# Kernel optimization log

Measured on AMD Instinct MI355X. Metric: run time of the kernel, lower is better.

Reference implementation:

```python
import jax, jax.numpy as jnp
import numpy as np

H = 256  # hidden size
I = 2    # input size / output size


def setup_inputs() -> dict:
    key = jax.random.key(0)
    ks = jax.random.split(key, 11)
    s1 = 1.0 / np.sqrt(H)
    u = lambda k, shape: jax.random.uniform(k, shape, jnp.float32, -s1, s1)
    return {
        "inputs": jax.random.normal(ks[0], (512, 256, I), jnp.float32),
        "W_ih1": u(ks[1], (4 * H, I)),
        "W_hh1": u(ks[2], (4 * H, H)),
        "b_ih1": u(ks[3], (4 * H,)),
        "b_hh1": u(ks[4], (4 * H,)),
        "W_ih2": u(ks[5], (4 * H, H)),
        "W_hh2": u(ks[6], (4 * H, H)),
        "b_ih2": u(ks[7], (4 * H,)),
        "b_hh2": u(ks[8], (4 * H,)),
        "W_lin": u(ks[9], (I, H)),
        "b_lin": u(ks[10], (I,)),
    }


def _lstm_cell(x, h, c, W_ih, W_hh, b_ih, b_hh):
    # PyTorch LSTMCell gate order: i, f, g, o
    gates = x @ W_ih.T + b_ih + h @ W_hh.T + b_hh  # (B, 4H)
    i, f, g, o = jnp.split(gates, 4, axis=-1)
    c_new = jax.nn.sigmoid(f) * c + jax.nn.sigmoid(i) * jnp.tanh(g)
    h_new = jax.nn.sigmoid(o) * jnp.tanh(c_new)
    return h_new, c_new


def reference(inputs, W_ih1, W_hh1, b_ih1, b_hh1, W_ih2, W_hh2, b_ih2, b_hh2,
              W_lin, b_lin):
    B = inputs.shape[0]
    xs = jnp.transpose(inputs, (1, 0, 2))  # (T, B, I)
    zeros = jnp.zeros((B, H), inputs.dtype)
    carry0 = (zeros, zeros, zeros, zeros)

    def step(carry, x_t):
        h1, c1, h2, c2 = carry
        # NOTE: the original clones/masks x_t into lstm_input_t but never
        # uses it — the cell consumes raw input_t, so we do the same.
        h1, c1 = _lstm_cell(x_t, h1, c1, W_ih1, W_hh1, b_ih1, b_hh1)
        h2, c2 = _lstm_cell(h1, h2, c2, W_ih2, W_hh2, b_ih2, b_hh2)
        y = h2 @ W_lin.T + b_lin  # (B, I)
        return (h1, c1, h2, c2), y

    _, ys = jax.lax.scan(step, carry0, xs)  # ys: (T, B, I)
    return jnp.transpose(ys, (1, 0, 2))  # (B, T, I)
```

## Files before the change

kernel.cpp:

```cpp
#include <hip/hip_runtime.h>


typedef float vf2 __attribute__((ext_vector_type(2)));
typedef float v4f __attribute__((ext_vector_type(4)));
typedef _Float16 vh4 __attribute__((ext_vector_type(4)));
typedef _Float16 vh8 __attribute__((ext_vector_type(8)));

#define NT 512
#define TSTEPS 256
#define NSF 144
#define NVPF 32
#define NLPF 16
#define FRB 1024
#define VPBASE (1152 * FRB)
#define LPBASE (1408 * FRB)
#define FS 393216

__global__ void prep_kernel(const float* __restrict__ W_ih1,
                            const float* __restrict__ W_hh1,
                            const float* __restrict__ b_ih1,
                            const float* __restrict__ b_hh1,
                            const float* __restrict__ W_ih2,
                            const float* __restrict__ W_hh2,
                            const float* __restrict__ b_ih2,
                            const float* __restrict__ b_hh2,
                            void* __restrict__ ws) {
    const int stride = gridDim.x * blockDim.x;
    const int idx = blockIdx.x * blockDim.x + threadIdx.x;
    _Float16* wh = (_Float16*)ws;
    float* wf = (float*)ws;
    for (int e = idx; e < 786432; e += stride) {
        int kb = e >> 9;
        int lane = (e & 511) >> 3, jj = e & 7;
        int w, rt, kt, m;
        if (kb < 1152) {
            w = kb / 144; int f = kb % 144;
            if (f < 64)       { m = 0; rt = f >> 3;        kt = f & 7; }
            else if (f < 128) { m = 1; rt = (f - 64) >> 3; kt = f & 7; }
            else { int q = f - 128; m = 2; rt = q >> 1; kt = (q & 1) ? 5 : 0; }
        } else if (kb < 1408) {
            int p2 = kb - 1152; w = p2 >> 5; int p = p2 & 31;
            m = 2; rt = p >> 2; kt = 1 + (p & 3);
        } else {
            int k3 = kb - 1408; w = k3 >> 4; int q = k3 & 15;
            m = 2; rt = q >> 1; kt = 6 + (q & 1);
        }
        int row = w * 128 + rt * 16 + (lane & 15);
        int k   = kt * 32 + ((lane >> 4) << 3) + jj;
        float v = (m == 0) ? W_hh1[row * 256 + k]
                : (m == 1) ? W_ih2[row * 256 + k]
                           : W_hh2[row * 256 + k];
        wh[e] = (_Float16)v;
    }
    for (int j = idx; j < 1024; j += stride) {
        wf[FS + j]        = W_ih1[j * 2 + 0];
        wf[FS + 1024 + j] = W_ih1[j * 2 + 1];
        wf[FS + 2048 + j] = b_ih1[j] + b_hh1[j];
        wf[FS + 3072 + j] = b_ih2[j] + b_hh2[j];
    }
}

__device__ __forceinline__ float sig_(float v) {
    return 1.f / (1.f + __expf(-v));
}
__device__ __forceinline__ float tanh_(float v) {
    return 1.f - 2.f / (__expf(2.f * v) + 1.f);
}
__device__ __forceinline__ v4f mfma16(vh8 a, vh8 b, v4f c) {
    return __builtin_amdgcn_mfma_f32_16x16x32_f16(a, b, c, 0, 0, 0);
}

#define BARRIER() __asm__ volatile("s_waitcnt lgkmcnt(0)\ns_barrier" ::: "memory")

__global__ __launch_bounds__(NT, 2) void lstm_kernel(
    const float* __restrict__ x,
    const void* __restrict__ ws,
    const float* __restrict__ W_lin,
    const float* __restrict__ b_lin,
    float* __restrict__ out)
{
    __shared__ float g1buf[2][1024];
    __shared__ float g2buf[2][1024];
    __shared__ __align__(16) _Float16 h1s[2][256];
    __shared__ __align__(16) _Float16 h2s[2][256];
    __shared__ __align__(16) char lds_park[NLPF * 8 * FRB];

    const int tid = threadIdx.x;
    const int lane = tid & 63, w = tid >> 6;
    const int u = tid & 255, bu = tid >> 8;
    const int b0 = blockIdx.x * 2;
    const char* wstream = (const char*)ws;
    const float* wf = (const float*)ws;
    const int l16 = lane * 16;

    float wxa[4], wxb[4], b1c[4], b2c[4];
    #pragma unroll
    for (int g = 0; g < 4; ++g) {
        int r = g * 256 + u;
        wxa[g] = wf[FS + r];        wxb[g] = wf[FS + 1024 + r];
        b1c[g] = wf[FS + 2048 + r]; b2c[g] = wf[FS + 3072 + r];
    }

    const int ob = (w >> 1) & 1, oo = w & 1;
    const float wl0 = W_lin[oo * 256 + 4 * lane + 0];
    const float wl1 = W_lin[oo * 256 + 4 * lane + 1];
    const float wl2 = W_lin[oo * 256 + 4 * lane + 2];
    const float wl3 = W_lin[oo * 256 + 4 * lane + 3];
    const float blin = b_lin[oo];

    ((_Float16*)h1s)[tid] = (_Float16)0.f;
    ((_Float16*)h2s)[tid] = (_Float16)0.f;
    g1buf[0][tid] = 0.f; g1buf[0][512 + tid] = 0.f;
    g1buf[1][tid] = 0.f; g1buf[1][512 + tid] = 0.f;

    float c1 = 0.f, c2 = 0.f;

    for (int q = 0; q < NLPF; ++q) {
        *(vh8*)&lds_park[(((q << 3) + w) << 10) + l16] =
            *(const vh8*)(wstream + LPBASE + (((w << 4) + q) << 10) + l16);
    }

    vh8 wreg[NVPF];
    #pragma unroll
    for (int p = 0; p < NVPF; ++p) {
        union { vh8 v; float f[4]; } tpk;
        tpk.v = *(const vh8*)(wstream + VPBASE + ((w * NVPF + p) << 10) + l16);
        asm volatile("" : "+v"(tpk.f[0]), "+v"(tpk.f[1]),
                          "+v"(tpk.f[2]), "+v"(tpk.f[3]));
        wreg[p] = tpk.v;
    }

    const char* wbase = wstream + (size_t)w * (NSF * FRB);
    int sp = 0;
    vh8 B0, B1, B2, B3, B4, B5, B6, B7;
    auto LDA = [&](vh8& d) {
        d = *(const vh8*)(wbase + sp + l16);
        sp += FRB; if (sp == NSF * FRB) sp = 0;
    };
    LDA(B0); LDA(B1); LDA(B2); LDA(B3);
    LDA(B4); LDA(B5); LDA(B6); LDA(B7);

    auto bfrag = [&](const _Float16 (*hp)[256], int kt) -> vh8 {
        return *(const vh8*)&hp[lane & 1][kt * 32 + ((lane >> 4) << 3)];
    };

    const int bx = b0 + bu;
    vf2 xv = *(const vf2*)(x + (size_t)bx * 512);

    __syncthreads();

    #pragma unroll 1
    for (int t = 0; t < TSTEPS; ++t) {
        {
            float p0 = g1buf[bu][u]       + b1c[0] + wxa[0] * xv.x + wxb[0] * xv.y;
            float p1 = g1buf[bu][256 + u] + b1c[1] + wxa[1] * xv.x + wxb[1] * xv.y;
            float p2 = g1buf[bu][512 + u] + b1c[2] + wxa[2] * xv.x + wxb[2] * xv.y;
            float p3 = g1buf[bu][768 + u] + b1c[3] + wxa[3] * xv.x + wxb[3] * xv.y;
            c1 = sig_(p1) * c1 + sig_(p0) * tanh_(p2);
            h1s[bu][u] = (_Float16)(sig_(p3) * tanh_(c1));
        }
        {
            const int tn = (t + 1) & (TSTEPS - 1);
            xv = *(const vf2*)(x + (size_t)bx * 512 + tn * 2);
        }
        BARRIER();

        if (t > 0 && w < 4) {
            vh4 hv = *(const vh4*)&h2s[ob][4 * lane];
            float s = (float)hv.x * wl0 + (float)hv.y * wl1
                    + (float)hv.z * wl2 + (float)hv.w * wl3;
            #pragma unroll
            for (int m = 32; m >= 1; m >>= 1) s += __shfl_xor(s, m, 64);
            if (lane == 0)
                out[(size_t)(b0 + ob) * 512 + (t - 1) * 2 + oo] = s + blin;
        }

        #pragma unroll 1
        for (int rt = 0; rt < 8; ++rt) {
            v4f acc = {0.f, 0.f, 0.f, 0.f};
            acc = mfma16(B0, bfrag(h1s, 0), acc); LDA(B0);
            acc = mfma16(B1, bfrag(h1s, 1), acc); LDA(B1);
            acc = mfma16(B2, bfrag(h1s, 2), acc); LDA(B2);
            acc = mfma16(B3, bfrag(h1s, 3), acc); LDA(B3);
            acc = mfma16(B4, bfrag(h1s, 4), acc); LDA(B4);
            acc = mfma16(B5, bfrag(h1s, 5), acc); LDA(B5);
            acc = mfma16(B6, bfrag(h1s, 6), acc); LDA(B6);
            acc = mfma16(B7, bfrag(h1s, 7), acc); LDA(B7);
            if ((lane & 15) < 2)
                *(v4f*)&g1buf[lane & 15][w * 128 + rt * 16 + ((lane >> 4) << 2)] = acc;
        }

        #pragma unroll 1
        for (int rt = 0; rt < 8; ++rt) {
            v4f acc = {0.f, 0.f, 0.f, 0.f};
            acc = mfma16(B0, bfrag(h1s, 0), acc); LDA(B0);
            acc = mfma16(B1, bfrag(h1s, 1), acc); LDA(B1);
            acc = mfma16(B2, bfrag(h1s, 2), acc); LDA(B2);
            acc = mfma16(B3, bfrag(h1s, 3), acc); LDA(B3);
            acc = mfma16(B4, bfrag(h1s, 4), acc); LDA(B4);
            acc = mfma16(B5, bfrag(h1s, 5), acc); LDA(B5);
            acc = mfma16(B6, bfrag(h1s, 6), acc); LDA(B6);
            acc = mfma16(B7, bfrag(h1s, 7), acc); LDA(B7);
            if ((lane & 15) < 2)
                *(v4f*)&g2buf[lane & 15][w * 128 + rt * 16 + ((lane >> 4) << 2)] = acc;
        }

#define P2B(RT, BA, BB)                                                        \
        {                                                                      \
            v4f acc = {0.f, 0.f, 0.f, 0.f};                                    \
            if ((lane & 15) < 2)                                               \
                acc = *(const v4f*)&g2buf[lane & 15]                           \
                        [w * 128 + RT * 16 + ((lane >> 4) << 2)];              \
            acc = mfma16(BA, bfrag(h2s, 0), acc); LDA(BA);                     \
            acc = mfma16(wreg[RT * 4 + 0], bfrag(h2s, 1), acc);                \
            acc = mfma16(wreg[RT * 4 + 1], bfrag(h2s, 2), acc);                \
            acc = mfma16(wreg[RT * 4 + 2], bfrag(h2s, 3), acc);                \
            acc = mfma16(wreg[RT * 4 + 3], bfrag(h2s, 4), acc);                \
            acc = mfma16(BB, bfrag(h2s, 5), acc); LDA(BB);                     \
            {                                                                  \
                vh8 A6 = *(const vh8*)                                         \
                    &lds_park[((((RT * 2 + 0) << 3) + w) << 10) + l16];        \
                acc = mfma16(A6, bfrag(h2s, 6), acc);                          \
            }                                                                  \
            {                                                                  \
                vh8 A7 = *(const vh8*)                                         \
                    &lds_park[((((RT * 2 + 1) << 3) + w) << 10) + l16];        \
                acc = mfma16(A7, bfrag(h2s, 7), acc);                          \
            }                                                                  \
            if ((lane & 15) < 2)                                               \
                *(v4f*)&g2buf[lane & 15]                                       \
                    [w * 128 + RT * 16 + ((lane >> 4) << 2)] = acc;            \
        }
        P2B(0, B0, B1) P2B(1, B2, B3) P2B(2, B4, B5) P2B(3, B6, B7)
        P2B(4, B0, B1) P2B(5, B2, B3) P2B(6, B4, B5) P2B(7, B6, B7)
#undef P2B
        BARRIER();

        {
            float q0 = g2buf[bu][u]       + b2c[0];
            float q1 = g2buf[bu][256 + u] + b2c[1];
            float q2 = g2buf[bu][512 + u] + b2c[2];
            float q3 = g2buf[bu][768 + u] + b2c[3];
            c2 = sig_(q1) * c2 + sig_(q0) * tanh_(q2);
            h2s[bu][u] = (_Float16)(sig_(q3) * tanh_(c2));
        }
    }

    BARRIER();
    if (w < 4) {
        vh4 hv = *(const vh4*)&h2s[ob][4 * lane];
        float s = (float)hv.x * wl0 + (float)hv.y * wl1
                + (float)hv.z * wl2 + (float)hv.w * wl3;
        #pragma unroll
        for (int m = 32; m >= 1; m >>= 1) s += __shfl_xor(s, m, 64);
        if (lane == 0)
            out[(size_t)(b0 + ob) * 512 + 255 * 2 + oo] = s + blin;
    }
}

extern "C" void kernel_launch(void* const* d_in, const int* in_sizes, int n_in,
                              void* d_out, int out_size, void* d_ws, size_t ws_size,
                              hipStream_t stream) {
    const float* x     = (const float*)d_in[0];
    const float* W_ih1 = (const float*)d_in[1];
    const float* W_hh1 = (const float*)d_in[2];
    const float* b_ih1 = (const float*)d_in[3];
    const float* b_hh1 = (const float*)d_in[4];
    const float* W_ih2 = (const float*)d_in[5];
    const float* W_hh2 = (const float*)d_in[6];
    const float* b_ih2 = (const float*)d_in[7];
    const float* b_hh2 = (const float*)d_in[8];
    const float* W_lin = (const float*)d_in[9];
    const float* b_lin = (const float*)d_in[10];
    float* out = (float*)d_out;

    prep_kernel<<<256, 256, 0, stream>>>(W_ih1, W_hh1, b_ih1, b_hh1,
                                         W_ih2, W_hh2, b_ih2, b_hh2, d_ws);
    lstm_kernel<<<256, NT, 0, stream>>>(x, d_ws, W_lin, b_lin, out);
}
```

Baseline: 2.705 ms.

## Process four batch rows per block and rebalance weight residency between LDS and stream

Each block now handles four batch elements instead of two, with 128 blocks instead of 256. The same streamed weight fragments feed MFMAs over more batch columns, so global weight traffic per batch element is halved. To fit the larger gate and hidden buffers in LDS, the parked W_hh2 tile for kt=7 moves back into the global stream, so the per-step stream grows from 144 to 152 fragments. Each thread now runs two LSTM cell updates per layer, and only half as many blocks are launched, which may leave CUs idle.

```diff
diff --git a/kernel.cpp b/kernel.cpp
--- a/kernel.cpp
+++ b/kernel.cpp
@@ -8,12 +8,12 @@
 
 #define NT 512
 #define TSTEPS 256
-#define NSF 144
+#define NSF 152
 #define NVPF 32
-#define NLPF 16
+#define NLPF 8
 #define FRB 1024
-#define VPBASE (1152 * FRB)
-#define LPBASE (1408 * FRB)
+#define VPBASE (1216 * FRB)
+#define LPBASE (1472 * FRB)
 #define FS 393216
 
 __global__ void prep_kernel(const float* __restrict__ W_ih1,
@@ -33,17 +33,20 @@
         int kb = e >> 9;
         int lane = (e & 511) >> 3, jj = e & 7;
         int w, rt, kt, m;
-        if (kb < 1152) {
-            w = kb / 144; int f = kb % 144;
+        if (kb < 1216) {
+            w = kb / 152; int f = kb % 152;
             if (f < 64)       { m = 0; rt = f >> 3;        kt = f & 7; }
             else if (f < 128) { m = 1; rt = (f - 64) >> 3; kt = f & 7; }
-            else { int q = f - 128; m = 2; rt = q >> 1; kt = (q & 1) ? 5 : 0; }
-        } else if (kb < 1408) {
-            int p2 = kb - 1152; w = p2 >> 5; int p = p2 & 31;
+            else {
+                int q = f - 128; m = 2; rt = q / 3; int pos = q % 3;
+                kt = (pos == 0) ? 0 : (pos == 1) ? 5 : 7;
+            }
+        } else if (kb < 1472) {
+            int p2 = kb - 1216; w = p2 >> 5; int p = p2 & 31;
             m = 2; rt = p >> 2; kt = 1 + (p & 3);
         } else {
-            int k3 = kb - 1408; w = k3 >> 4; int q = k3 & 15;
-            m = 2; rt = q >> 1; kt = 6 + (q & 1);
+            int k3 = kb - 1472; w = k3 >> 3; int q = k3 & 7;
+            m = 2; rt = q; kt = 6;
         }
         int row = w * 128 + rt * 16 + (lane & 15);
         int k   = kt * 32 + ((lane >> 4) << 3) + jj;
@@ -79,16 +82,16 @@
     const float* __restrict__ b_lin,
     float* __restrict__ out)
 {
-    __shared__ float g1buf[2][1024];
-    __shared__ float g2buf[2][1024];
-    __shared__ __align__(16) _Float16 h1s[2][256];
-    __shared__ __align__(16) _Float16 h2s[2][256];
+    __shared__ float g1buf[4][1024];
+    __shared__ float g2buf[4][1024];
+    __shared__ __align__(16) _Float16 h1s[4][288];
+    __shared__ __align__(16) _Float16 h2s[4][288];
     __shared__ __align__(16) char lds_park[NLPF * 8 * FRB];
 
     const int tid = threadIdx.x;
     const int lane = tid & 63, w = tid >> 6;
     const int u = tid & 255, bu = tid >> 8;
-    const int b0 = blockIdx.x * 2;
+    const int b0 = blockIdx.x * 4;
     const char* wstream = (const char*)ws;
     const float* wf = (const float*)ws;
     const int l16 = lane * 16;
@@ -101,23 +104,24 @@
         b1c[g] = wf[FS + 2048 + r]; b2c[g] = wf[FS + 3072 + r];
     }
 
-    const int ob = (w >> 1) & 1, oo = w & 1;
+    const int ob = w >> 1, oo = w & 1;
     const float wl0 = W_lin[oo * 256 + 4 * lane + 0];
     const float wl1 = W_lin[oo * 256 + 4 * lane + 1];
     const float wl2 = W_lin[oo * 256 + 4 * lane + 2];
     const float wl3 = W_lin[oo * 256 + 4 * lane + 3];
     const float blin = b_lin[oo];
 
-    ((_Float16*)h1s)[tid] = (_Float16)0.f;
-    ((_Float16*)h2s)[tid] = (_Float16)0.f;
-    g1buf[0][tid] = 0.f; g1buf[0][512 + tid] = 0.f;
-    g1buf[1][tid] = 0.f; g1buf[1][512 + tid] = 0.f;
-
-    float c1 = 0.f, c2 = 0.f;
+    for (int i = tid; i < 4 * 288; i += NT) {
+        ((_Float16*)h1s)[i] = (_Float16)0.f;
+        ((_Float16*)h2s)[i] = (_Float16)0.f;
+    }
+    for (int i = tid; i < 4096; i += NT) ((float*)g1buf)[i] = 0.f;
+
+    float c1a = 0.f, c1b = 0.f, c2a = 0.f, c2b = 0.f;
 
     for (int q = 0; q < NLPF; ++q) {
         *(vh8*)&lds_park[(((q << 3) + w) << 10) + l16] =
-            *(const vh8*)(wstream + LPBASE + (((w << 4) + q) << 10) + l16);
+            *(const vh8*)(wstream + LPBASE + (((w << 3) + q) << 10) + l16);
     }
 
     vh8 wreg[NVPF];
@@ -140,32 +144,40 @@
     LDA(B0); LDA(B1); LDA(B2); LDA(B3);
     LDA(B4); LDA(B5); LDA(B6); LDA(B7);
 
-    auto bfrag = [&](const _Float16 (*hp)[256], int kt) -> vh8 {
-        return *(const vh8*)&hp[lane & 1][kt * 32 + ((lane >> 4) << 3)];
+    auto bfrag = [&](const _Float16 (*hp)[288], int kt) -> vh8 {
+        return *(const vh8*)&hp[lane & 3][kt * 32 + ((lane >> 4) << 3)];
     };
 
-    const int bx = b0 + bu;
-    vf2 xv = *(const vf2*)(x + (size_t)bx * 512);
+    const int bxa = b0 + bu, bxb = b0 + bu + 2;
+    vf2 xva = *(const vf2*)(x + (size_t)bxa * 512);
+    vf2 xvb = *(const vf2*)(x + (size_t)bxb * 512);
 
     __syncthreads();
 
     #pragma unroll 1
     for (int t = 0; t < TSTEPS; ++t) {
         {
-            float p0 = g1buf[bu][u]       + b1c[0] + wxa[0] * xv.x + wxb[0] * xv.y;
-            float p1 = g1buf[bu][256 + u] + b1c[1] + wxa[1] * xv.x + wxb[1] * xv.y;
-            float p2 = g1buf[bu][512 + u] + b1c[2] + wxa[2] * xv.x + wxb[2] * xv.y;
-            float p3 = g1buf[bu][768 + u] + b1c[3] + wxa[3] * xv.x + wxb[3] * xv.y;
-            c1 = sig_(p1) * c1 + sig_(p0) * tanh_(p2);
-            h1s[bu][u] = (_Float16)(sig_(p3) * tanh_(c1));
+            float p0 = g1buf[bu][u]       + b1c[0] + wxa[0] * xva.x + wxb[0] * xva.y;
+            float p1 = g1buf[bu][256 + u] + b1c[1] + wxa[1] * xva.x + wxb[1] * xva.y;
+            float p2 = g1buf[bu][512 + u] + b1c[2] + wxa[2] * xva.x + wxb[2] * xva.y;
+            float p3 = g1buf[bu][768 + u] + b1c[3] + wxa[3] * xva.x + wxb[3] * xva.y;
+            c1a = sig_(p1) * c1a + sig_(p0) * tanh_(p2);
+            h1s[bu][u] = (_Float16)(sig_(p3) * tanh_(c1a));
+            float q0 = g1buf[bu + 2][u]       + b1c[0] + wxa[0] * xvb.x + wxb[0] * xvb.y;
+            float q1 = g1buf[bu + 2][256 + u] + b1c[1] + wxa[1] * xvb.x + wxb[1] * xvb.y;
+            float q2 = g1buf[bu + 2][512 + u] + b1c[2] + wxa[2] * xvb.x + wxb[2] * xvb.y;
+            float q3 = g1buf[bu + 2][768 + u] + b1c[3] + wxa[3] * xvb.x + wxb[3] * xvb.y;
+            c1b = sig_(q1) * c1b + sig_(q0) * tanh_(q2);
+            h1s[bu + 2][u] = (_Float16)(sig_(q3) * tanh_(c1b));
         }
         {
             const int tn = (t + 1) & (TSTEPS - 1);
-            xv = *(const vf2*)(x + (size_t)bx * 512 + tn * 2);
+            xva = *(const vf2*)(x + (size_t)bxa * 512 + tn * 2);
+            xvb = *(const vf2*)(x + (size_t)bxb * 512 + tn * 2);
         }
         BARRIER();
 
-        if (t > 0 && w < 4) {
+        if (t > 0) {
             vh4 hv = *(const vh4*)&h2s[ob][4 * lane];
             float s = (float)hv.x * wl0 + (float)hv.y * wl1
                     + (float)hv.z * wl2 + (float)hv.w * wl3;
@@ -186,7 +198,7 @@
             acc = mfma16(B5, bfrag(h1s, 5), acc); LDA(B5);
             acc = mfma16(B6, bfrag(h1s, 6), acc); LDA(B6);
             acc = mfma16(B7, bfrag(h1s, 7), acc); LDA(B7);
-            if ((lane & 15) < 2)
+            if ((lane & 15) < 4)
                 *(v4f*)&g1buf[lane & 15][w * 128 + rt * 16 + ((lane >> 4) << 2)] = acc;
         }
 
@@ -201,14 +213,14 @@
             acc = mfma16(B5, bfrag(h1s, 5), acc); LDA(B5);
             acc = mfma16(B6, bfrag(h1s, 6), acc); LDA(B6);
             acc = mfma16(B7, bfrag(h1s, 7), acc); LDA(B7);
-            if ((lane & 15) < 2)
+            if ((lane & 15) < 4)
                 *(v4f*)&g2buf[lane & 15][w * 128 + rt * 16 + ((lane >> 4) << 2)] = acc;
         }
 
-#define P2B(RT, BA, BB)                                                        \
+#define P2B(RT, BA, BB, BC)                                                    \
         {                                                                      \
             v4f acc = {0.f, 0.f, 0.f, 0.f};                                    \
-            if ((lane & 15) < 2)                                               \
+            if ((lane & 15) < 4)                                               \
                 acc = *(const v4f*)&g2buf[lane & 15]                           \
                         [w * 128 + RT * 16 + ((lane >> 4) << 2)];              \
             acc = mfma16(BA, bfrag(h2s, 0), acc); LDA(BA);                     \
@@ -219,35 +231,38 @@
             acc = mfma16(BB, bfrag(h2s, 5), acc); LDA(BB);                     \
             {                                                                  \
                 vh8 A6 = *(const vh8*)                                         \
-                    &lds_park[((((RT * 2 + 0) << 3) + w) << 10) + l16];        \
+                    &lds_park[(((RT << 3) + w) << 10) + l16];                  \
                 acc = mfma16(A6, bfrag(h2s, 6), acc);                          \
             }                                                                  \
-            {                                                                  \
-                vh8 A7 = *(const vh8*)                                         \
-                    &lds_park[((((RT * 2 + 1) << 3) + w) << 10) + l16];        \
-                acc = mfma16(A7, bfrag(h2s, 7), acc);                          \
-            }                                                                  \
-            if ((lane & 15) < 2)                                               \
+            acc = mfma16(BC, bfrag(h2s, 7), acc); LDA(BC);                     \
+            if ((lane & 15) < 4)                                               \
                 *(v4f*)&g2buf[lane & 15]                                       \
                     [w * 128 + RT * 16 + ((lane >> 4) << 2)] = acc;            \
         }
-        P2B(0, B0, B1) P2B(1, B2, B3) P2B(2, B4, B5) P2B(3, B6, B7)
-        P2B(4, B0, B1) P2B(5, B2, B3) P2B(6, B4, B5) P2B(7, B6, B7)
+        P2B(0, B0, B1, B2) P2B(1, B3, B4, B5) P2B(2, B6, B7, B0)
+        P2B(3, B1, B2, B3) P2B(4, B4, B5, B6) P2B(5, B7, B0, B1)
+        P2B(6, B2, B3, B4) P2B(7, B5, B6, B7)
 #undef P2B
         BARRIER();
 
         {
-            float q0 = g2buf[bu][u]       + b2c[0];
-            float q1 = g2buf[bu][256 + u] + b2c[1];
-            float q2 = g2buf[bu][512 + u] + b2c[2];
-            float q3 = g2buf[bu][768 + u] + b2c[3];
-            c2 = sig_(q1) * c2 + sig_(q0) * tanh_(q2);
-            h2s[bu][u] = (_Float16)(sig_(q3) * tanh_(c2));
+            float p0 = g2buf[bu][u]       + b2c[0];
+            float p1 = g2buf[bu][256 + u] + b2c[1];
+            float p2 = g2buf[bu][512 + u] + b2c[2];
+            float p3 = g2buf[bu][768 + u] + b2c[3];
+            c2a = sig_(p1) * c2a + sig_(p0) * tanh_(p2);
+            h2s[bu][u] = (_Float16)(sig_(p3) * tanh_(c2a));
+            float q0 = g2buf[bu + 2][u]       + b2c[0];
+            float q1 = g2buf[bu + 2][256 + u] + b2c[1];
+            float q2 = g2buf[bu + 2][512 + u] + b2c[2];
+            float q3 = g2buf[bu + 2][768 + u] + b2c[3];
+            c2b = sig_(q1) * c2b + sig_(q0) * tanh_(q2);
+            h2s[bu + 2][u] = (_Float16)(sig_(q3) * tanh_(c2b));
         }
     }
 
     BARRIER();
-    if (w < 4) {
+    {
         vh4 hv = *(const vh4*)&h2s[ob][4 * lane];
         float s = (float)hv.x * wl0 + (float)hv.y * wl1
                 + (float)hv.z * wl2 + (float)hv.w * wl3;
@@ -276,5 +291,5 @@
 
     prep_kernel<<<256, 256, 0, stream>>>(W_ih1, W_hh1, b_ih1, b_hh1,
                                          W_ih2, W_hh2, b_ih2, b_hh2, d_ws);
-    lstm_kernel<<<256, NT, 0, stream>>>(x, d_ws, W_lin, b_lin, out);
-}
+    lstm_kernel<<<128, NT, 0, stream>>>(x, d_ws, W_lin, b_lin, out);
+}
```

Result: slower. 2.875 ms (+6.3%).

## Deepen streamed weight prefetch to 16 registers and rebalance register/LDS parking

Applied to the files above, without the earlier changes.

Doubles the ring of streamed weight fragments held in VGPRs from 8 to 16 so that global loads are issued further ahead of their MFMA use. The gate loops now process two row tiles per iteration with two independent accumulators. To free registers, fewer W_hh2 fragments are kept resident in VGPRs (24 instead of 32) and fewer in LDS (8 instead of 16), so more are streamed from global memory each step, and the prep kernel's fragment layout is changed to match. This adds per-step global/L2 traffic and register pressure in exchange for more latency hiding and more instruction-level parallelism.

```diff
diff --git a/kernel.cpp b/kernel.cpp
--- a/kernel.cpp
+++ b/kernel.cpp
@@ -8,12 +8,12 @@
 
 #define NT 512
 #define TSTEPS 256
-#define NSF 144
-#define NVPF 32
-#define NLPF 16
+#define NSF 160
+#define NVPF 24
+#define NLPF 8
 #define FRB 1024
-#define VPBASE (1152 * FRB)
-#define LPBASE (1408 * FRB)
+#define VPBASE (1280 * FRB)
+#define LPBASE (1472 * FRB)
 #define FS 393216
 
 __global__ void prep_kernel(const float* __restrict__ W_ih1,
@@ -33,17 +33,20 @@
         int kb = e >> 9;
         int lane = (e & 511) >> 3, jj = e & 7;
         int w, rt, kt, m;
-        if (kb < 1152) {
-            w = kb / 144; int f = kb % 144;
+        if (kb < 1280) {
+            w = kb / 160; int f = kb % 160;
             if (f < 64)       { m = 0; rt = f >> 3;        kt = f & 7; }
             else if (f < 128) { m = 1; rt = (f - 64) >> 3; kt = f & 7; }
-            else { int q = f - 128; m = 2; rt = q >> 1; kt = (q & 1) ? 5 : 0; }
-        } else if (kb < 1408) {
-            int p2 = kb - 1152; w = p2 >> 5; int p = p2 & 31;
-            m = 2; rt = p >> 2; kt = 1 + (p & 3);
+            else {
+                int q = f - 128; m = 2; rt = q >> 2; int pos = q & 3;
+                kt = (pos == 0) ? 0 : (pos == 1) ? 4 : (pos == 2) ? 5 : 7;
+            }
+        } else if (kb < 1472) {
+            int p2 = kb - 1280; w = p2 / 24; int p = p2 % 24;
+            m = 2; rt = p / 3; kt = 1 + p % 3;
         } else {
-            int k3 = kb - 1408; w = k3 >> 4; int q = k3 & 15;
-            m = 2; rt = q >> 1; kt = 6 + (q & 1);
+            int k3 = kb - 1472; w = k3 >> 3; int q = k3 & 7;
+            m = 2; rt = q; kt = 6;
         }
         int row = w * 128 + rt * 16 + (lane & 15);
         int k   = kt * 32 + ((lane >> 4) << 3) + jj;
@@ -117,7 +120,7 @@
 
     for (int q = 0; q < NLPF; ++q) {
         *(vh8*)&lds_park[(((q << 3) + w) << 10) + l16] =
-            *(const vh8*)(wstream + LPBASE + (((w << 4) + q) << 10) + l16);
+            *(const vh8*)(wstream + LPBASE + (((w << 3) + q) << 10) + l16);
     }
 
     vh8 wreg[NVPF];
@@ -132,13 +135,13 @@
 
     const char* wbase = wstream + (size_t)w * (NSF * FRB);
     int sp = 0;
-    vh8 B0, B1, B2, B3, B4, B5, B6, B7;
+    vh8 B0, B1, B2, B3, B4, B5, B6, B7, B8, B9, B10, B11, B12, B13, B14, B15;
     auto LDA = [&](vh8& d) {
         d = *(const vh8*)(wbase + sp + l16);
         sp += FRB; if (sp == NSF * FRB) sp = 0;
     };
-    LDA(B0); LDA(B1); LDA(B2); LDA(B3);
-    LDA(B4); LDA(B5); LDA(B6); LDA(B7);
+    LDA(B0); LDA(B1); LDA(B2);  LDA(B3);  LDA(B4);  LDA(B5);  LDA(B6);  LDA(B7);
+    LDA(B8); LDA(B9); LDA(B10); LDA(B11); LDA(B12); LDA(B13); LDA(B14); LDA(B15);
 
     auto bfrag = [&](const _Float16 (*hp)[256], int kt) -> vh8 {
         return *(const vh8*)&hp[lane & 1][kt * 32 + ((lane >> 4) << 3)];
@@ -176,63 +179,81 @@
         }
 
         #pragma unroll 1
-        for (int rt = 0; rt < 8; ++rt) {
-            v4f acc = {0.f, 0.f, 0.f, 0.f};
-            acc = mfma16(B0, bfrag(h1s, 0), acc); LDA(B0);
-            acc = mfma16(B1, bfrag(h1s, 1), acc); LDA(B1);
-            acc = mfma16(B2, bfrag(h1s, 2), acc); LDA(B2);
-            acc = mfma16(B3, bfrag(h1s, 3), acc); LDA(B3);
-            acc = mfma16(B4, bfrag(h1s, 4), acc); LDA(B4);
-            acc = mfma16(B5, bfrag(h1s, 5), acc); LDA(B5);
-            acc = mfma16(B6, bfrag(h1s, 6), acc); LDA(B6);
-            acc = mfma16(B7, bfrag(h1s, 7), acc); LDA(B7);
-            if ((lane & 15) < 2)
-                *(v4f*)&g1buf[lane & 15][w * 128 + rt * 16 + ((lane >> 4) << 2)] = acc;
+        for (int rp = 0; rp < 4; ++rp) {
+            v4f a0 = {0.f, 0.f, 0.f, 0.f}, a1 = {0.f, 0.f, 0.f, 0.f};
+            a0 = mfma16(B0, bfrag(h1s, 0), a0); LDA(B0);
+            a0 = mfma16(B1, bfrag(h1s, 1), a0); LDA(B1);
+            a0 = mfma16(B2, bfrag(h1s, 2), a0); LDA(B2);
+            a0 = mfma16(B3, bfrag(h1s, 3), a0); LDA(B3);
+            a0 = mfma16(B4, bfrag(h1s, 4), a0); LDA(B4);
+            a0 = mfma16(B5, bfrag(h1s, 5), a0); LDA(B5);
+            a0 = mfma16(B6, bfrag(h1s, 6), a0); LDA(B6);
+            a0 = mfma16(B7, bfrag(h1s, 7), a0); LDA(B7);
+            a1 = mfma16(B8,  bfrag(h1s, 0), a1); LDA(B8);
+            a1 = mfma16(B9,  bfrag(h1s, 1), a1); LDA(B9);
+            a1 = mfma16(B10, bfrag(h1s, 2), a1); LDA(B10);
+            a1 = mfma16(B11, bfrag(h1s, 3), a1); LDA(B11);
+            a1 = mfma16(B12, bfrag(h1s, 4), a1); LDA(B12);
+            a1 = mfma16(B13, bfrag(h1s, 5), a1); LDA(B13);
+            a1 = mfma16(B14, bfrag(h1s, 6), a1); LDA(B14);
+            a1 = mfma16(B15, bfrag(h1s, 7), a1); LDA(B15);
+            if ((lane & 15) < 2) {
+                *(v4f*)&g1buf[lane & 15][w * 128 + (2 * rp) * 16 + ((lane >> 4) << 2)] = a0;
+                *(v4f*)&g1buf[lane & 15][w * 128 + (2 * rp + 1) * 16 + ((lane >> 4) << 2)] = a1;
+            }
         }
 
         #pragma unroll 1
-        for (int rt = 0; rt < 8; ++rt) {
-            v4f acc = {0.f, 0.f, 0.f, 0.f};
-            acc = mfma16(B0, bfrag(h1s, 0), acc); LDA(B0);
-            acc = mfma16(B1, bfrag(h1s, 1), acc); LDA(B1);
-            acc = mfma16(B2, bfrag(h1s, 2), acc); LDA(B2);
-            acc = mfma16(B3, bfrag(h1s, 3), acc); LDA(B3);
-            acc = mfma16(B4, bfrag(h1s, 4), acc); LDA(B4);
-            acc = mfma16(B5, bfrag(h1s, 5), acc); LDA(B5);
-            acc = mfma16(B6, bfrag(h1s, 6), acc); LDA(B6);
-            acc = mfma16(B7, bfrag(h1s, 7), acc); LDA(B7);
-            if ((lane & 15) < 2)
-                *(v4f*)&g2buf[lane & 15][w * 128 + rt * 16 + ((lane >> 4) << 2)] = acc;
-        }
-
-#define P2B(RT, BA, BB)                                                        \
+        for (int rp = 0; rp < 4; ++rp) {
+            v4f a0 = {0.f, 0.f, 0.f, 0.f}, a1 = {0.f, 0.f, 0.f, 0.f};
+            a0 = mfma16(B0, bfrag(h1s, 0), a0); LDA(B0);
+            a0 = mfma16(B1, bfrag(h1s, 1), a0); LDA(B1);
+            a0 = mfma16(B2, bfrag(h1s, 2), a0); LDA(B2);
+            a0 = mfma16(B3, bfrag(h1s, 3), a0); LDA(B3);
+            a0 = mfma16(B4, bfrag(h1s, 4), a0); LDA(B4);
+            a0 = mfma16(B5, bfrag(h1s, 5), a0); LDA(B5);
+            a0 = mfma16(B6, bfrag(h1s, 6), a0); LDA(B6);
+            a0 = mfma16(B7, bfrag(h1s, 7), a0); LDA(B7);
+            a1 = mfma16(B8,  bfrag(h1s, 0), a1); LDA(B8);
+            a1 = mfma16(B9,  bfrag(h1s, 1), a1); LDA(B9);
+            a1 = mfma16(B10, bfrag(h1s, 2), a1); LDA(B10);
+            a1 = mfma16(B11, bfrag(h1s, 3), a1); LDA(B11);
+            a1 = mfma16(B12, bfrag(h1s, 4), a1); LDA(B12);
+            a1 = mfma16(B13, bfrag(h1s, 5), a1); LDA(B13);
+            a1 = mfma16(B14, bfrag(h1s, 6), a1); LDA(B14);
+            a1 = mfma16(B15, bfrag(h1s, 7), a1); LDA(B15);
+            if ((lane & 15) < 2) {
+                *(v4f*)&g2buf[lane & 15][w * 128 + (2 * rp) * 16 + ((lane >> 4) << 2)] = a0;
+                *(v4f*)&g2buf[lane & 15][w * 128 + (2 * rp + 1) * 16 + ((lane >> 4) << 2)] = a1;
+            }
+        }
+
+#define P2B(RT, BA, BB, BC, BD)                                                \
         {                                                                      \
             v4f acc = {0.f, 0.f, 0.f, 0.f};                                    \
             if ((lane & 15) < 2)                                               \
                 acc = *(const v4f*)&g2buf[lane & 15]                           \
                         [w * 128 + RT * 16 + ((lane >> 4) << 2)];              \
             acc = mfma16(BA, bfrag(h2s, 0), acc); LDA(BA);                     \
-            acc = mfma16(wreg[RT * 4 + 0], bfrag(h2s, 1), acc);                \
-            acc = mfma16(wreg[RT * 4 + 1], bfrag(h2s, 2), acc);                \
-            acc = mfma16(wreg[RT * 4 + 2], bfrag(h2s, 3), acc);                \
-            acc = mfma16(wreg[RT * 4 + 3], bfrag(h2s, 4), acc);                \
-            acc = mfma16(BB, bfrag(h2s, 5), acc); LDA(BB);                     \
+            acc = mfma16(wreg[RT * 3 + 0], bfrag(h2s, 1), acc);                \
+            acc = mfma16(wreg[RT * 3 + 1], bfrag(h2s, 2), acc);                \
+            acc = mfma16(wreg[RT * 3 + 2], bfrag(h2s, 3), acc);                \
+            acc = mfma16(BB, bfrag(h2s, 4), acc); LDA(BB);                     \
+            acc = mfma16(BC, bfrag(h2s, 5), acc); LDA(BC);                     \
             {                                                                  \
                 vh8 A6 = *(const vh8*)                                         \
-                    &lds_park[((((RT * 2 + 0) << 3) + w) << 10) + l16];        \
+                    &lds_park[(((RT << 3) + w) << 10) + l16];                  \
                 acc = mfma16(A6, bfrag(h2s, 6), acc);                          \
             }                                                                  \
-            {                                                                  \
-                vh8 A7 = *(const vh8*)                                         \
-                    &lds_park[((((RT * 2 + 1) << 3) + w) << 10) + l16];        \
-                acc = mfma16(A7, bfrag(h2s, 7), acc);                          \
-            }                                                                  \
+            acc = mfma16(BD, bfrag(h2s, 7), acc); LDA(BD);                     \
             if ((lane & 15) < 2)                                               \
                 *(v4f*)&g2buf[lane & 15]                                       \
                     [w * 128 + RT * 16 + ((lane >> 4) << 2)] = acc;            \
         }
-        P2B(0, B0, B1) P2B(1, B2, B3) P2B(2, B4, B5) P2B(3, B6, B7)
-        P2B(4, B0, B1) P2B(5, B2, B3) P2B(6, B4, B5) P2B(7, B6, B7)
+        P2B(0, B0,  B1,  B2,  B3)  P2B(1, B4,  B5,  B6,  B7)
+        P2B(2, B8,  B9,  B10, B11) P2B(3, B12, B13, B14, B15)
+        P2B(4, B0,  B1,  B2,  B3)  P2B(5, B4,  B5,  B6,  B7)
+        P2B(6, B8,  B9,  B10, B11) P2B(7, B12, B13, B14, B15)
 #undef P2B
         BARRIER();
 
```

Measured after the change: 2.910 ms. 7.6% more time.

## Hoist h fragments into registers and shrink register-parked weight set

Applied to the files above, without the earlier changes.

The B-operand fragments of h1 and h2 are now loaded from LDS once per phase into eight registers and reused across all row tiles, instead of being reloaded for every MFMA. To pay for those extra registers, the number of W_hh2 fragments kept permanently in registers drops from 4 to 3 per row tile. The extra fragment is streamed from global memory through the rotating B0–B7 buffers, and the prep-kernel layout changes to match. This cuts LDS reads but adds streamed weight traffic and a more complex buffer rotation.

```diff
diff --git a/kernel.cpp b/kernel.cpp
--- a/kernel.cpp
+++ b/kernel.cpp
@@ -8,11 +8,11 @@
 
 #define NT 512
 #define TSTEPS 256
-#define NSF 144
-#define NVPF 32
+#define NSF 152
+#define NVPF 24
 #define NLPF 16
 #define FRB 1024
-#define VPBASE (1152 * FRB)
+#define VPBASE (1216 * FRB)
 #define LPBASE (1408 * FRB)
 #define FS 393216
 
@@ -33,14 +33,17 @@
         int kb = e >> 9;
         int lane = (e & 511) >> 3, jj = e & 7;
         int w, rt, kt, m;
-        if (kb < 1152) {
-            w = kb / 144; int f = kb % 144;
+        if (kb < 1216) {
+            w = kb / 152; int f = kb % 152;
             if (f < 64)       { m = 0; rt = f >> 3;        kt = f & 7; }
             else if (f < 128) { m = 1; rt = (f - 64) >> 3; kt = f & 7; }
-            else { int q = f - 128; m = 2; rt = q >> 1; kt = (q & 1) ? 5 : 0; }
+            else {
+                int q = f - 128; m = 2; rt = q / 3; int pos = q % 3;
+                kt = (pos == 0) ? 0 : (pos == 1) ? 4 : 5;
+            }
         } else if (kb < 1408) {
-            int p2 = kb - 1152; w = p2 >> 5; int p = p2 & 31;
-            m = 2; rt = p >> 2; kt = 1 + (p & 3);
+            int p2 = kb - 1216; w = p2 / 24; int p = p2 % 24;
+            m = 2; rt = p / 3; kt = 1 + p % 3;
         } else {
             int k3 = kb - 1408; w = k3 >> 4; int q = k3 & 15;
             m = 2; rt = q >> 1; kt = 6 + (q & 1);
@@ -175,17 +178,22 @@
                 out[(size_t)(b0 + ob) * 512 + (t - 1) * 2 + oo] = s + blin;
         }
 
+        vh8 hf0 = bfrag(h1s, 0), hf1 = bfrag(h1s, 1);
+        vh8 hf2 = bfrag(h1s, 2), hf3 = bfrag(h1s, 3);
+        vh8 hf4 = bfrag(h1s, 4), hf5 = bfrag(h1s, 5);
+        vh8 hf6 = bfrag(h1s, 6), hf7 = bfrag(h1s, 7);
+
         #pragma unroll 1
         for (int rt = 0; rt < 8; ++rt) {
             v4f acc = {0.f, 0.f, 0.f, 0.f};
-            acc = mfma16(B0, bfrag(h1s, 0), acc); LDA(B0);
-            acc = mfma16(B1, bfrag(h1s, 1), acc); LDA(B1);
-            acc = mfma16(B2, bfrag(h1s, 2), acc); LDA(B2);
-            acc = mfma16(B3, bfrag(h1s, 3), acc); LDA(B3);
-            acc = mfma16(B4, bfrag(h1s, 4), acc); LDA(B4);
-            acc = mfma16(B5, bfrag(h1s, 5), acc); LDA(B5);
-            acc = mfma16(B6, bfrag(h1s, 6), acc); LDA(B6);
-            acc = mfma16(B7, bfrag(h1s, 7), acc); LDA(B7);
+            acc = mfma16(B0, hf0, acc); LDA(B0);
+            acc = mfma16(B1, hf1, acc); LDA(B1);
+            acc = mfma16(B2, hf2, acc); LDA(B2);
+            acc = mfma16(B3, hf3, acc); LDA(B3);
+            acc = mfma16(B4, hf4, acc); LDA(B4);
+            acc = mfma16(B5, hf5, acc); LDA(B5);
+            acc = mfma16(B6, hf6, acc); LDA(B6);
+            acc = mfma16(B7, hf7, acc); LDA(B7);
             if ((lane & 15) < 2)
                 *(v4f*)&g1buf[lane & 15][w * 128 + rt * 16 + ((lane >> 4) << 2)] = acc;
         }
@@ -193,46 +201,52 @@
         #pragma unroll 1
         for (int rt = 0; rt < 8; ++rt) {
             v4f acc = {0.f, 0.f, 0.f, 0.f};
-            acc = mfma16(B0, bfrag(h1s, 0), acc); LDA(B0);
-            acc = mfma16(B1, bfrag(h1s, 1), acc); LDA(B1);
-            acc = mfma16(B2, bfrag(h1s, 2), acc); LDA(B2);
-            acc = mfma16(B3, bfrag(h1s, 3), acc); LDA(B3);
-            acc = mfma16(B4, bfrag(h1s, 4), acc); LDA(B4);
-            acc = mfma16(B5, bfrag(h1s, 5), acc); LDA(B5);
-            acc = mfma16(B6, bfrag(h1s, 6), acc); LDA(B6);
-            acc = mfma16(B7, bfrag(h1s, 7), acc); LDA(B7);
+            acc = mfma16(B0, hf0, acc); LDA(B0);
+            acc = mfma16(B1, hf1, acc); LDA(B1);
+            acc = mfma16(B2, hf2, acc); LDA(B2);
+            acc = mfma16(B3, hf3, acc); LDA(B3);
+            acc = mfma16(B4, hf4, acc); LDA(B4);
+            acc = mfma16(B5, hf5, acc); LDA(B5);
+            acc = mfma16(B6, hf6, acc); LDA(B6);
+            acc = mfma16(B7, hf7, acc); LDA(B7);
             if ((lane & 15) < 2)
                 *(v4f*)&g2buf[lane & 15][w * 128 + rt * 16 + ((lane >> 4) << 2)] = acc;
         }
 
-#define P2B(RT, BA, BB)                                                        \
+        hf0 = bfrag(h2s, 0); hf1 = bfrag(h2s, 1);
+        hf2 = bfrag(h2s, 2); hf3 = bfrag(h2s, 3);
+        hf4 = bfrag(h2s, 4); hf5 = bfrag(h2s, 5);
+        hf6 = bfrag(h2s, 6); hf7 = bfrag(h2s, 7);
+
+#define P2B(RT, BA, BB, BC)                                                    \
         {                                                                      \
             v4f acc = {0.f, 0.f, 0.f, 0.f};                                    \
             if ((lane & 15) < 2)                                               \
                 acc = *(const v4f*)&g2buf[lane & 15]                           \
                         [w * 128 + RT * 16 + ((lane >> 4) << 2)];              \
-            acc = mfma16(BA, bfrag(h2s, 0), acc); LDA(BA);                     \
-            acc = mfma16(wreg[RT * 4 + 0], bfrag(h2s, 1), acc);                \
-            acc = mfma16(wreg[RT * 4 + 1], bfrag(h2s, 2), acc);                \
-            acc = mfma16(wreg[RT * 4 + 2], bfrag(h2s, 3), acc);                \
-            acc = mfma16(wreg[RT * 4 + 3], bfrag(h2s, 4), acc);                \
-            acc = mfma16(BB, bfrag(h2s, 5), acc); LDA(BB);                     \
+            acc = mfma16(BA, hf0, acc); LDA(BA);                               \
+            acc = mfma16(wreg[RT * 3 + 0], hf1, acc);                          \
+            acc = mfma16(wreg[RT * 3 + 1], hf2, acc);                          \
+            acc = mfma16(wreg[RT * 3 + 2], hf3, acc);                          \
+            acc = mfma16(BB, hf4, acc); LDA(BB);                               \
+            acc = mfma16(BC, hf5, acc); LDA(BC);                               \
             {                                                                  \
                 vh8 A6 = *(const vh8*)                                         \
                     &lds_park[((((RT * 2 + 0) << 3) + w) << 10) + l16];        \
-                acc = mfma16(A6, bfrag(h2s, 6), acc);                          \
+                acc = mfma16(A6, hf6, acc);                                    \
             }                                                                  \
             {                                                                  \
                 vh8 A7 = *(const vh8*)                                         \
                     &lds_park[((((RT * 2 + 1) << 3) + w) << 10) + l16];        \
-                acc = mfma16(A7, bfrag(h2s, 7), acc);                          \
+                acc = mfma16(A7, hf7, acc);                                    \
             }                                                                  \
             if ((lane & 15) < 2)                                               \
                 *(v4f*)&g2buf[lane & 15]                                       \
                     [w * 128 + RT * 16 + ((lane >> 4) << 2)] = acc;            \
         }
-        P2B(0, B0, B1) P2B(1, B2, B3) P2B(2, B4, B5) P2B(3, B6, B7)
-        P2B(4, B0, B1) P2B(5, B2, B3) P2B(6, B4, B5) P2B(7, B6, B7)
+        P2B(0, B0, B1, B2) P2B(1, B3, B4, B5) P2B(2, B6, B7, B0)
+        P2B(3, B1, B2, B3) P2B(4, B4, B5, B6) P2B(5, B7, B0, B1)
+        P2B(6, B2, B3, B4) P2B(7, B5, B6, B7)
 #undef P2B
         BARRIER();
 
```

After: 2.748 ms. No clear change (+1.6%).
